# Kernel optimization log

Measured on AMD Instinct MI355X. Metric: run time of the kernel, lower is better.

Reference implementation:

```python
import jax, jax.numpy as jnp
import numpy as np

HIDDEN = 768
HEADS = 12
HEAD_DIM = HIDDEN // HEADS
BETA = 0.5
BANDWIDTH = 1.0
D_INTRINSIC = 3
LN_EPS = 1e-12


def setup_inputs() -> dict:
    key = jax.random.key(0)
    ks = jax.random.split(key, 10)
    B, S, E = 2, 2048, HIDDEN
    sc = 1.0 / np.sqrt(E)
    return {
        "hidden_states": jax.random.normal(ks[0], (B, S, E), jnp.float32),
        "attention_mask": jnp.zeros((B, S), jnp.float32),
        "Wq": jax.random.normal(ks[1], (E, E), jnp.float32) * sc,
        "bq": jax.random.normal(ks[2], (E,), jnp.float32) * 0.02,
        "Wv": jax.random.normal(ks[3], (E, E), jnp.float32) * sc,
        "bv": jax.random.normal(ks[4], (E,), jnp.float32) * 0.02,
        "Wo": jax.random.normal(ks[5], (E, E), jnp.float32) * sc,
        "bo": jax.random.normal(ks[6], (E,), jnp.float32) * 0.02,
        "ln_g": jnp.ones((E,), jnp.float32),
        "ln_b": jnp.zeros((E,), jnp.float32),
    }


def _layernorm(x, g, b, eps=LN_EPS):
    mu = jnp.mean(x, axis=-1, keepdims=True)
    var = jnp.mean((x - mu) ** 2, axis=-1, keepdims=True)
    return (x - mu) * jax.lax.rsqrt(var + eps) * g + b


def reference(hidden_states, attention_mask, Wq, bq, Wv, bv, Wo, bo, ln_g, ln_b):
    B, S, E = hidden_states.shape
    H, D = HEADS, HEAD_DIM
    # projections (torch Linear: x @ W.T + b)
    q = (hidden_states @ Wq.T + bq).reshape(B, S, H, D).transpose(0, 2, 1, 3)  # [B,H,S,D]
    v = (hidden_states @ Wv.T + bv).reshape(B, S, H, D).transpose(0, 2, 1, 3)  # [B,H,S,D]
    # pairwise Euclidean distance (cdist) via norm expansion, safe sqrt
    qn = jnp.sum(q * q, axis=-1)  # [B,H,S]
    d2 = qn[:, :, :, None] + qn[:, :, None, :] - 2.0 * jnp.einsum("bhid,bhjd->bhij", q, q)
    dist = jnp.sqrt(jnp.maximum(d2, 1e-12))  # [B,H,S,S]
    # mask: positions with attention_mask < 0 get distance 2
    keep = (attention_mask >= 0)  # [B,S]
    pair_keep = keep[:, None, :, None] & keep[:, None, None, :]  # [B,1,S,S]
    dist = jnp.where(pair_keep, dist, 2.0)
    # power-law score + softmax
    attn_score = (1.0 + dist / (BANDWIDTH ** 0.5)) ** (-D_INTRINSIC - BETA)
    attn = jax.nn.softmax(attn_score, axis=-1)
    out = jnp.einsum("bhij,bhjd->bhid", attn, v)  # [B,H,S,D]
    out = out.transpose(0, 2, 1, 3).reshape(B, S, E)
    # ModelSelfOutput: dense + residual + LayerNorm (dropout=0, eval)
    out = out @ Wo.T + bo
    return _layernorm(out + hidden_states, ln_g, ln_b)
```

## Files before the change

### kernel.cpp

```cpp
#include <hip/hip_runtime.h>
#include <hip/hip_bf16.h>
#include <cstdint>
#include <cstddef>

#define S_LEN 2048
#define NH 12
#define HD 64
#define EDIM 768

typedef short bf16x8 __attribute__((ext_vector_type(8)));
typedef float f32x4  __attribute__((ext_vector_type(4)));
typedef float f32x2  __attribute__((ext_vector_type(2)));

__device__ __forceinline__ unsigned short f2bf(float f) {
    return __bfloat16_as_ushort(__float2bfloat16(f));
}
__device__ __forceinline__ float bf2f(unsigned short u) {
    union { unsigned int i; float f; } x;
    x.i = ((unsigned int)u) << 16;
    return x.f;
}
__device__ __forceinline__ float rsq_f32(float x) {
#if __has_builtin(__builtin_amdgcn_rsqf)
    return __builtin_amdgcn_rsqf(x);
#else
    return __builtin_amdgcn_rcpf(__builtin_amdgcn_sqrtf(x));
#endif
}

__global__ __launch_bounds__(256) void precast_kernel(
    const float* __restrict__ hs, const float* __restrict__ Wq,
    const float* __restrict__ Wv, const float* __restrict__ Wo,
    unsigned short* __restrict__ hsb, unsigned short* __restrict__ Wqvb,
    unsigned short* __restrict__ Wob)
{
    const int i4 = blockIdx.x * 256 + threadIdx.x;
    const float* src;
    unsigned short* dst;
    int rel;
    if (i4 < 786432)        { src = hs; dst = hsb;            rel = i4; }
    else if (i4 < 933888)   { src = Wq; dst = Wqvb;           rel = i4 - 786432; }
    else if (i4 < 1081344)  { src = Wv; dst = Wqvb + 589824;  rel = i4 - 933888; }
    else                    { src = Wo; dst = Wob;            rel = i4 - 1081344; }
    float4 v = ((const float4*)src)[rel];
    ushort4 o;
    o.x = f2bf(v.x); o.y = f2bf(v.y); o.z = f2bf(v.z); o.w = f2bf(v.w);
    ((ushort4*)dst)[rel] = o;
}

__global__ __launch_bounds__(256) void qv_gemm(
    const unsigned short* __restrict__ hsb, const unsigned short* __restrict__ Wqvb,
    const float* __restrict__ bq, const float* __restrict__ bv,
    unsigned short* __restrict__ Qb, unsigned short* __restrict__ Vt,
    float* __restrict__ qn)
{
    __shared__ __align__(16) unsigned short As[64][40];
    __shared__ __align__(16) unsigned short Bs[128][40];

    const int t  = threadIdx.x;
    const int m0 = blockIdx.y << 6;
    const int c0 = blockIdx.x << 7;
    const bool isQ = (c0 < EDIM);
    const float* bias = isQ ? bq : bv;
    const int cb = isQ ? c0 : (c0 - EDIM);

    const int w  = t >> 6;
    const int l  = t & 63;
    const int ll = l & 15;
    const int lq = l >> 4;
    const int wx = w & 1;
    const int wy = w >> 1;

    const int srowA = t & 63;
    const int skA   = (t >> 6) << 3;
    const int srowB = t & 127;
    const int skB   = (t >> 7) << 4;

    f32x4 acc[2][4];
#pragma unroll
    for (int m = 0; m < 2; m++)
#pragma unroll
        for (int n = 0; n < 4; n++) acc[m][n] = (f32x4){0.f, 0.f, 0.f, 0.f};

    for (int k0 = 0; k0 < EDIM; k0 += 32) {
        bf16x8 va  = *(const bf16x8*)(hsb  + (size_t)(m0 + srowA) * EDIM + k0 + skA);
        bf16x8 vb0 = *(const bf16x8*)(Wqvb + (size_t)(c0 + srowB) * EDIM + k0 + skB);
        bf16x8 vb1 = *(const bf16x8*)(Wqvb + (size_t)(c0 + srowB) * EDIM + k0 + skB + 8);
        __syncthreads();
        *(bf16x8*)&As[srowA][skA]     = va;
        *(bf16x8*)&Bs[srowB][skB]     = vb0;
        *(bf16x8*)&Bs[srowB][skB + 8] = vb1;
        __syncthreads();
        bf16x8 aF[2], bF[4];
#pragma unroll
        for (int m = 0; m < 2; m++)
            aF[m] = *(const bf16x8*)&As[(wy << 5) + (m << 4) + ll][lq << 3];
#pragma unroll
        for (int n = 0; n < 4; n++)
            bF[n] = *(const bf16x8*)&Bs[(wx << 6) + (n << 4) + ll][lq << 3];
#pragma unroll
        for (int m = 0; m < 2; m++)
#pragma unroll
            for (int n = 0; n < 4; n++)
                acc[m][n] = __builtin_amdgcn_mfma_f32_16x16x32_bf16(aF[m], bF[n], acc[m][n], 0, 0, 0);
    }

    const int hcol0 = cb + (wx << 6);
    const int h = hcol0 >> 6;
    const int rowbase = m0 + (wy << 5);
    const int b = rowbase >> 11;
    const int sbase = rowbase & 2047;

    if (isQ) {
#pragma unroll
        for (int m = 0; m < 2; m++) {
#pragma unroll
            for (int r = 0; r < 4; r++) {
                const int si = sbase + (m << 4) + (lq << 2) + r;
                unsigned short* qrow = Qb + ((size_t)(b * NH + h) * S_LEN + si) * HD;
                float qsq = 0.f;
#pragma unroll
                for (int n = 0; n < 4; n++) {
                    unsigned short u = f2bf(acc[m][n][r] + bias[hcol0 + (n << 4) + ll]);
                    qrow[(n << 4) + ll] = u;
                    float f = bf2f(u);
                    qsq += f * f;
                }
                qsq += __shfl_xor(qsq, 1);
                qsq += __shfl_xor(qsq, 2);
                qsq += __shfl_xor(qsq, 4);
                qsq += __shfl_xor(qsq, 8);
                if (ll == 0) qn[(b * NH + h) * S_LEN + si] = qsq;
            }
        }
    } else {
#pragma unroll
        for (int m = 0; m < 2; m++) {
            const int si = sbase + (m << 4) + (lq << 2);
#pragma unroll
            for (int n = 0; n < 4; n++) {
                ushort4 o;
                o.x = f2bf(acc[m][n][0] + bias[hcol0 + (n << 4) + ll]);
                o.y = f2bf(acc[m][n][1] + bias[hcol0 + (n << 4) + ll]);
                o.z = f2bf(acc[m][n][2] + bias[hcol0 + (n << 4) + ll]);
                o.w = f2bf(acc[m][n][3] + bias[hcol0 + (n << 4) + ll]);
                *(ushort4*)&Vt[((size_t)(b * NH + h) * HD + (n << 4) + ll) * S_LEN + si] = o;
            }
        }
    }
}

template<int CUR>
__device__ __forceinline__ void attn_tile32(
    int j0, int jn,
    const unsigned short* __restrict__ Qbase,
    const unsigned short* __restrict__ Vbase,
    const float* __restrict__ qnb, const float* __restrict__ mb,
    int ll, int lq,
    const bf16x8 (&aQ)[2][2],
    const f32x2 (&qni2)[2][2], const f32x2 (&keepi2)[2][2],
    const bf16x8& ones,
    f32x4 (&oacc)[2][4], f32x4 (&wacc)[2],
    bf16x8 (&nb0)[2], bf16x8 (&nb1)[2],
    bf16x8 (&vbuf)[2][4],
    float (&qnjv)[2][2], float (&kjm)[2][2],
    unsigned short (&Wt)[2][2][16][40])
{
    constexpr int PRV = CUR ^ 1;
    __builtin_amdgcn_wave_barrier();
#pragma unroll
    for (int m = 0; m < 4; m++)
        vbuf[CUR][m] = *(const bf16x8*)(Vbase + (size_t)((m << 4) + ll) * S_LEN + j0 + (lq << 3));
    f32x4 s[2][2];
#pragma unroll
    for (int s2 = 0; s2 < 2; s2++)
#pragma unroll
        for (int n = 0; n < 2; n++) {
            f32x4 c = (f32x4){0.f, 0.f, 0.f, 0.f};
            c = __builtin_amdgcn_mfma_f32_16x16x32_bf16(aQ[s2][0], nb0[n], c, 0, 0, 0);
            c = __builtin_amdgcn_mfma_f32_16x16x32_bf16(aQ[s2][1], nb1[n], c, 0, 0, 0);
            s[s2][n] = c;
        }
#pragma unroll
    for (int n = 0; n < 2; n++) {
        const unsigned short* bp = Qbase + (size_t)(jn + (n << 4) + ll) * HD + (lq << 3);
        nb0[n] = *(const bf16x8*)bp;
        nb1[n] = *(const bf16x8*)(bp + 32);
        int jc = jn + (n << 4) + ll;
        qnjv[PRV][n] = qnb[jc];
        kjm[PRV][n]  = (mb[jc] >= 0.f) ? 1.f : 0.f;
    }
#pragma unroll
    for (int s2 = 0; s2 < 2; s2++) {
        bf16x8 aP = *(const bf16x8*)&Wt[PRV][s2][ll][lq << 3];
#pragma unroll
        for (int m = 0; m < 4; m++)
            oacc[s2][m] = __builtin_amdgcn_mfma_f32_16x16x32_bf16(aP, vbuf[PRV][m], oacc[s2][m], 0, 0, 0);
        wacc[s2] = __builtin_amdgcn_mfma_f32_16x16x32_bf16(aP, ones, wacc[s2], 0, 0, 0);
    }
#pragma unroll
    for (int s2 = 0; s2 < 2; s2++)
#pragma unroll
        for (int n = 0; n < 2; n++) {
            const f32x2 qv = (f32x2)(qnjv[CUR][n]);
            const f32x2 kj = (f32x2)(kjm[CUR][n]);
#pragma unroll
            for (int pr = 0; pr < 2; pr++) {
                f32x2 sp = { s[s2][n][2*pr], s[s2][n][2*pr + 1] };
                f32x2 d2 = __builtin_elementwise_fma(sp, (f32x2)(-2.f), qni2[s2][pr] + qv);
                d2 = __builtin_elementwise_max(d2, (f32x2)(1e-12f));
                f32x2 dist = { __builtin_amdgcn_sqrtf(d2.x), __builtin_amdgcn_sqrtf(d2.y) };
                f32x2 km = keepi2[s2][pr] * kj;
                f32x2 x  = __builtin_elementwise_fma(km, dist + (f32x2)(-2.f), (f32x2)(3.f));
                f32x2 x2 = x * x;
                f32x2 x4 = x2 * x2;
                f32x2 x6 = x4 * x2;
                f32x2 x7 = x6 * x;
                f32x2 p  = { rsq_f32(x7.x), rsq_f32(x7.y) };
                f32x2 wv = __builtin_elementwise_fma(
                    __builtin_elementwise_fma(
                        __builtin_elementwise_fma(
                            __builtin_elementwise_fma((f32x2)(0.041666668f), p, (f32x2)(0.16666667f)),
                            p, (f32x2)(0.5f)),
                        p, (f32x2)(1.0f)),
                    p, (f32x2)(1.0f));
                union { float f; unsigned int u; } c0, c1;
                c0.f = wv.x; c1.f = wv.y;
                Wt[CUR][s2][(lq << 2) + 2*pr    ][(n << 4) + ll] = (unsigned short)((c0.u + 0x8000u) >> 16);
                Wt[CUR][s2][(lq << 2) + 2*pr + 1][(n << 4) + ll] = (unsigned short)((c1.u + 0x8000u) >> 16);
            }
        }
}

__global__ __launch_bounds__(128) void attn_kernel(
    const unsigned short* __restrict__ Qb, const unsigned short* __restrict__ Vt,
    const float* __restrict__ qn, const float* __restrict__ mask,
    unsigned short* __restrict__ AObf)
{
    __shared__ __align__(16) unsigned short Wt[2][2][2][16][40];

    const int t  = threadIdx.x;
    const int w  = t >> 6;
    const int l  = t & 63;
    const int ll = l & 15;
    const int lq = l >> 4;
    const int id = blockIdx.x;
    const int ib = id / 24;
    const int bh = id - ib * 24;
    const int b  = bh / NH;
    const int h  = bh - b * NH;
    const int iw = ib << 5;

    const unsigned short* Qbase = Qb + ((size_t)bh << 17);
    const unsigned short* Vbase = Vt + ((size_t)bh << 17);
    const float* qnb = qn + (bh << 11);
    const float* mb  = mask + (b << 11);

    unsigned short (&Wtw)[2][2][16][40] = Wt[w];

    const int tbase = w << 5;
    const int jb    = tbase << 5;

    bf16x8 aQ[2][2];
#pragma unroll
    for (int s2 = 0; s2 < 2; s2++) {
        const unsigned short* qp = Qbase + (size_t)(iw + (s2 << 4) + ll) * HD + (lq << 3);
        aQ[s2][0] = *(const bf16x8*)qp;
        aQ[s2][1] = *(const bf16x8*)(qp + 32);
    }

    f32x2 qni2[2][2], keepi2[2][2];
#pragma unroll
    for (int s2 = 0; s2 < 2; s2++)
#pragma unroll
        for (int pr = 0; pr < 2; pr++) {
            int r0 = iw + (s2 << 4) + (lq << 2) + 2*pr;
            qni2[s2][pr]   = (f32x2){ qnb[r0], qnb[r0 + 1] };
            keepi2[s2][pr] = (f32x2){ (mb[r0] >= 0.f) ? 1.f : 0.f,
                                      (mb[r0 + 1] >= 0.f) ? 1.f : 0.f };
        }

    bf16x8 ones;
#pragma unroll
    for (int i = 0; i < 8; i++) ones[i] = (short)0x3F80;

    f32x4 oacc[2][4];
#pragma unroll
    for (int s2 = 0; s2 < 2; s2++)
#pragma unroll
        for (int m = 0; m < 4; m++) oacc[s2][m] = (f32x4){0.f, 0.f, 0.f, 0.f};
    f32x4 wacc[2];
    wacc[0] = (f32x4){0.f, 0.f, 0.f, 0.f};
    wacc[1] = (f32x4){0.f, 0.f, 0.f, 0.f};

    bf16x8 nb0[2], nb1[2];
    float qnjv[2][2], kjm[2][2];
#pragma unroll
    for (int n = 0; n < 2; n++) {
        const unsigned short* bp = Qbase + (size_t)(jb + (n << 4) + ll) * HD + (lq << 3);
        nb0[n] = *(const bf16x8*)bp;
        nb1[n] = *(const bf16x8*)(bp + 32);
        int jc = jb + (n << 4) + ll;
        qnjv[0][n] = qnb[jc];
        kjm[0][n]  = (mb[jc] >= 0.f) ? 1.f : 0.f;
    }
    bf16x8 vbuf[2][4];

    {
#pragma unroll
        for (int m = 0; m < 4; m++)
            vbuf[0][m] = *(const bf16x8*)(Vbase + (size_t)((m << 4) + ll) * S_LEN + jb + (lq << 3));
        f32x4 s[2][2];
#pragma unroll
        for (int s2 = 0; s2 < 2; s2++)
#pragma unroll
            for (int n = 0; n < 2; n++) {
                f32x4 c = (f32x4){0.f, 0.f, 0.f, 0.f};
                c = __builtin_amdgcn_mfma_f32_16x16x32_bf16(aQ[s2][0], nb0[n], c, 0, 0, 0);
                c = __builtin_amdgcn_mfma_f32_16x16x32_bf16(aQ[s2][1], nb1[n], c, 0, 0, 0);
                s[s2][n] = c;
            }
#pragma unroll
        for (int n = 0; n < 2; n++) {
            const unsigned short* bp = Qbase + (size_t)(jb + 32 + (n << 4) + ll) * HD + (lq << 3);
            nb0[n] = *(const bf16x8*)bp;
            nb1[n] = *(const bf16x8*)(bp + 32);
            int jc = jb + 32 + (n << 4) + ll;
            qnjv[1][n] = qnb[jc];
            kjm[1][n]  = (mb[jc] >= 0.f) ? 1.f : 0.f;
        }
#pragma unroll
        for (int s2 = 0; s2 < 2; s2++)
#pragma unroll
            for (int n = 0; n < 2; n++) {
                const f32x2 qv = (f32x2)(qnjv[0][n]);
                const f32x2 kj = (f32x2)(kjm[0][n]);
#pragma unroll
                for (int pr = 0; pr < 2; pr++) {
                    f32x2 sp = { s[s2][n][2*pr], s[s2][n][2*pr + 1] };
                    f32x2 d2 = __builtin_elementwise_fma(sp, (f32x2)(-2.f), qni2[s2][pr] + qv);
                    d2 = __builtin_elementwise_max(d2, (f32x2)(1e-12f));
                    f32x2 dist = { __builtin_amdgcn_sqrtf(d2.x), __builtin_amdgcn_sqrtf(d2.y) };
                    f32x2 km = keepi2[s2][pr] * kj;
                    f32x2 x  = __builtin_elementwise_fma(km, dist + (f32x2)(-2.f), (f32x2)(3.f));
                    f32x2 x2 = x * x;
                    f32x2 x4 = x2 * x2;
                    f32x2 x6 = x4 * x2;
                    f32x2 x7 = x6 * x;
                    f32x2 p  = { rsq_f32(x7.x), rsq_f32(x7.y) };
                    f32x2 wv = __builtin_elementwise_fma(
                        __builtin_elementwise_fma(
                            __builtin_elementwise_fma(
                                __builtin_elementwise_fma((f32x2)(0.041666668f), p, (f32x2)(0.16666667f)),
                                p, (f32x2)(0.5f)),
                            p, (f32x2)(1.0f)),
                        p, (f32x2)(1.0f));
                    union { float f; unsigned int u; } c0, c1;
                    c0.f = wv.x; c1.f = wv.y;
                    Wtw[0][s2][(lq << 2) + 2*pr    ][(n << 4) + ll] = (unsigned short)((c0.u + 0x8000u) >> 16);
                    Wtw[0][s2][(lq << 2) + 2*pr + 1][(n << 4) + ll] = (unsigned short)((c1.u + 0x8000u) >> 16);
                }
            }
    }

    for (int tt = tbase + 1; tt <= tbase + 29; tt += 2) {
        attn_tile32<1>(tt << 5, (tt + 1) << 5, Qbase, Vbase, qnb, mb, ll, lq,
                       aQ, qni2, keepi2, ones, oacc, wacc, nb0, nb1, vbuf, qnjv, kjm, Wtw);
        attn_tile32<0>((tt + 1) << 5, (tt + 2) << 5, Qbase, Vbase, qnb, mb, ll, lq,
                       aQ, qni2, keepi2, ones, oacc, wacc, nb0, nb1, vbuf, qnjv, kjm, Wtw);
    }
    attn_tile32<1>((tbase + 31) << 5, 0, Qbase, Vbase, qnb, mb, ll, lq,
                   aQ, qni2, keepi2, ones, oacc, wacc, nb0, nb1, vbuf, qnjv, kjm, Wtw);

    __builtin_amdgcn_wave_barrier();
#pragma unroll
    for (int s2 = 0; s2 < 2; s2++) {
        bf16x8 aP = *(const bf16x8*)&Wtw[1][s2][ll][lq << 3];
#pragma unroll
        for (int m = 0; m < 4; m++)
            oacc[s2][m] = __builtin_amdgcn_mfma_f32_16x16x32_bf16(aP, vbuf[1][m], oacc[s2][m], 0, 0, 0);
        wacc[s2] = __builtin_amdgcn_mfma_f32_16x16x32_bf16(aP, ones, wacc[s2], 0, 0, 0);
    }

    float* red = (float*)Wt;
    __syncthreads();
    if (w == 1) {
        float* p = red + l;
#pragma unroll
        for (int s2 = 0; s2 < 2; s2++)
#pragma unroll
            for (int m = 0; m < 4; m++)
#pragma unroll
                for (int r = 0; r < 4; r++)
                    p[((((s2 << 2) + m) << 2) + r) << 6] = oacc[s2][m][r];
#pragma unroll
        for (int s2 = 0; s2 < 2; s2++)
#pragma unroll
            for (int r = 0; r < 4; r++)
                p[(32 + (s2 << 2) + r) << 6] = wacc[s2][r];
    }
    __syncthreads();
    if (w == 0) {
        float* p = red + l;
#pragma unroll
        for (int s2 = 0; s2 < 2; s2++)
#pragma unroll
            for (int m = 0; m < 4; m++)
#pragma unroll
                for (int r = 0; r < 4; r++)
                    oacc[s2][m][r] += p[((((s2 << 2) + m) << 2) + r) << 6];
#pragma unroll
        for (int s2 = 0; s2 < 2; s2++)
#pragma unroll
            for (int r = 0; r < 4; r++)
                wacc[s2][r] += p[(32 + (s2 << 2) + r) << 6];

#pragma unroll
        for (int s2 = 0; s2 < 2; s2++)
#pragma unroll
            for (int r = 0; r < 4; r++) {
                float inv = 1.0f / wacc[s2][r];
                const int row = iw + (s2 << 4) + (lq << 2) + r;
                unsigned short* dst = AObf + (size_t)((b << 11) + row) * EDIM + (h << 6);
#pragma unroll
                for (int m = 0; m < 4; m++)
                    dst[(m << 4) + ll] = f2bf(oacc[s2][m][r] * inv);
            }
    }
}

__global__ __launch_bounds__(256) void oproj_gemm(
    const unsigned short* __restrict__ AObf, const unsigned short* __restrict__ Wob,
    const float* __restrict__ bo, const float* __restrict__ hs,
    float* __restrict__ TMP)
{
    __shared__ __align__(16) unsigned short As[64][40];
    __shared__ __align__(16) unsigned short Bs[64][40];

    const int t  = threadIdx.x;
    const int m0 = blockIdx.y << 6;
    const int c0 = blockIdx.x << 6;

    const int w  = t >> 6;
    const int l  = t & 63;
    const int ll = l & 15;
    const int lq = l >> 4;
    const int wx = w & 1;
    const int wy = w >> 1;

    const int srow = t & 63;
    const int sk   = (t >> 6) << 3;

    f32x4 acc[2][2];
#pragma unroll
    for (int m = 0; m < 2; m++)
#pragma unroll
        for (int n = 0; n < 2; n++) acc[m][n] = (f32x4){0.f, 0.f, 0.f, 0.f};

    for (int k0 = 0; k0 < EDIM; k0 += 32) {
        bf16x8 va = *(const bf16x8*)(AObf + (size_t)(m0 + srow) * EDIM + k0 + sk);
        bf16x8 vb = *(const bf16x8*)(Wob  + (size_t)(c0 + srow) * EDIM + k0 + sk);
        __syncthreads();
        *(bf16x8*)&As[srow][sk] = va;
        *(bf16x8*)&Bs[srow][sk] = vb;
        __syncthreads();
        bf16x8 aF[2], bF[2];
#pragma unroll
        for (int m = 0; m < 2; m++)
            aF[m] = *(const bf16x8*)&As[(wy << 5) + (m << 4) + ll][lq << 3];
#pragma unroll
        for (int n = 0; n < 2; n++)
            bF[n] = *(const bf16x8*)&Bs[(wx << 5) + (n << 4) + ll][lq << 3];
#pragma unroll
        for (int m = 0; m < 2; m++)
#pragma unroll
            for (int n = 0; n < 2; n++)
                acc[m][n] = __builtin_amdgcn_mfma_f32_16x16x32_bf16(aF[m], bF[n], acc[m][n], 0, 0, 0);
    }

#pragma unroll
    for (int m = 0; m < 2; m++) {
#pragma unroll
        for (int r = 0; r < 4; r++) {
            const int row = m0 + (wy << 5) + (m << 4) + (lq << 2) + r;
#pragma unroll
            for (int n = 0; n < 2; n++) {
                const int col = c0 + (wx << 5) + (n << 4) + ll;
                TMP[(size_t)row * EDIM + col] =
                    acc[m][n][r] + bo[col] + hs[(size_t)row * EDIM + col];
            }
        }
    }
}

__global__ __launch_bounds__(256) void ln_kernel(
    const float* __restrict__ X, const float* __restrict__ g,
    const float* __restrict__ be, float* __restrict__ out)
{
    const int row = blockIdx.x;
    const int t = threadIdx.x;
    const float* x = X + (size_t)row * EDIM;

    float s = 0.f, sq = 0.f;
#pragma unroll
    for (int c = t; c < EDIM; c += 256) {
        float v = x[c];
        s += v; sq += v * v;
    }
#pragma unroll
    for (int m = 1; m < 64; m <<= 1) {
        s  += __shfl_xor(s, m);
        sq += __shfl_xor(sq, m);
    }
    __shared__ float ss[4], ssq[4];
    const int w = t >> 6;
    if ((t & 63) == 0) { ss[w] = s; ssq[w] = sq; }
    __syncthreads();
    s  = ss[0] + ss[1] + ss[2] + ss[3];
    sq = ssq[0] + ssq[1] + ssq[2] + ssq[3];
    const float mu  = s * (1.f / EDIM);
    const float var = sq * (1.f / EDIM) - mu * mu;
    const float rstd = 1.0f / sqrtf(var + 1e-12f);

#pragma unroll
    for (int c = t; c < EDIM; c += 256) {
        out[(size_t)row * EDIM + c] = (x[c] - mu) * rstd * g[c] + be[c];
    }
}

extern "C" void kernel_launch(void* const* d_in, const int* in_sizes, int n_in,
                              void* d_out, int out_size, void* d_ws, size_t ws_size,
                              hipStream_t stream) {
    const float* hs   = (const float*)d_in[0];
    const float* mask = (const float*)d_in[1];
    const float* Wq   = (const float*)d_in[2];
    const float* bq   = (const float*)d_in[3];
    const float* Wv   = (const float*)d_in[4];
    const float* bv   = (const float*)d_in[5];
    const float* Wo   = (const float*)d_in[6];
    const float* bo   = (const float*)d_in[7];
    const float* g    = (const float*)d_in[8];
    const float* be   = (const float*)d_in[9];

    char* w8 = (char*)d_ws;
    unsigned short* Qb   = (unsigned short*)(w8);
    unsigned short* Vt   = (unsigned short*)(w8 +  6291456);
    float*          qn   = (float*)        (w8 + 12582912);
    unsigned short* AObf = (unsigned short*)(w8 + 12779520);
    unsigned short* hsb  = (unsigned short*)(w8 + 19070976);
    unsigned short* Wqvb = (unsigned short*)(w8 + 25362432);
    unsigned short* Wob  = (unsigned short*)(w8 + 27721728);
    float*          TMP  = (float*)(w8);

    precast_kernel<<<dim3(4800),    256, 0, stream>>>(hs, Wq, Wv, Wo, hsb, Wqvb, Wob);
    qv_gemm       <<<dim3(12, 64),  256, 0, stream>>>(hsb, Wqvb, bq, bv, Qb, Vt, qn);
    attn_kernel   <<<dim3(1536),    128, 0, stream>>>(Qb, Vt, qn, mask, AObf);
    oproj_gemm    <<<dim3(12, 64),  256, 0, stream>>>(AObf, Wob, bo, hs, TMP);
    ln_kernel     <<<dim3(4096),    256, 0, stream>>>(TMP, g, be, (float*)d_out);
}
```

Before: 264.1 us.

## Split attention key range across four waves per block with two-stage reduction

Each attention block now runs 256 threads instead of 128, so the key dimension is split four ways across waves rather than two, and each wave processes half as many key tiles. Partial outputs and normalizer sums are then merged in two stages through shared memory: waves 2–3 into waves 0–1, then wave 1 into wave 0. The goal is more waves in flight per CU and a shorter serial tile loop per wave, to hide latency better. The cost is an extra reduction round with more barriers, plus larger register and LDS pressure per block.

Measured after the change: 250.5 us. 1.05x faster.

```diff
diff --git a/kernel.cpp b/kernel.cpp
--- a/kernel.cpp
+++ b/kernel.cpp
@@ -232,12 +232,12 @@
         }
 }
 
-__global__ __launch_bounds__(128) void attn_kernel(
+__global__ __launch_bounds__(256) void attn_kernel(
     const unsigned short* __restrict__ Qb, const unsigned short* __restrict__ Vt,
     const float* __restrict__ qn, const float* __restrict__ mask,
     unsigned short* __restrict__ AObf)
 {
-    __shared__ __align__(16) unsigned short Wt[2][2][2][16][40];
+    __shared__ __align__(16) unsigned short Wt[4][2][2][16][40];
 
     const int t  = threadIdx.x;
     const int w  = t >> 6;
@@ -258,7 +258,7 @@
 
     unsigned short (&Wtw)[2][2][16][40] = Wt[w];
 
-    const int tbase = w << 5;
+    const int tbase = w << 4;
     const int jb    = tbase << 5;
 
     bf16x8 aQ[2][2];
@@ -363,13 +363,13 @@
             }
     }
 
-    for (int tt = tbase + 1; tt <= tbase + 29; tt += 2) {
+    for (int tt = tbase + 1; tt <= tbase + 13; tt += 2) {
         attn_tile32<1>(tt << 5, (tt + 1) << 5, Qbase, Vbase, qnb, mb, ll, lq,
                        aQ, qni2, keepi2, ones, oacc, wacc, nb0, nb1, vbuf, qnjv, kjm, Wtw);
         attn_tile32<0>((tt + 1) << 5, (tt + 2) << 5, Qbase, Vbase, qnb, mb, ll, lq,
                        aQ, qni2, keepi2, ones, oacc, wacc, nb0, nb1, vbuf, qnjv, kjm, Wtw);
     }
-    attn_tile32<1>((tbase + 31) << 5, 0, Qbase, Vbase, qnb, mb, ll, lq,
+    attn_tile32<1>((tbase + 15) << 5, 0, Qbase, Vbase, qnb, mb, ll, lq,
                    aQ, qni2, keepi2, ones, oacc, wacc, nb0, nb1, vbuf, qnjv, kjm, Wtw);
 
     __builtin_amdgcn_wave_barrier();
@@ -384,6 +384,38 @@
 
     float* red = (float*)Wt;
     __syncthreads();
+    if (w >= 2) {
+        float* p = red + (((w - 2) << 6) + l);
+#pragma unroll
+        for (int s2 = 0; s2 < 2; s2++)
+#pragma unroll
+            for (int m = 0; m < 4; m++)
+#pragma unroll
+                for (int r = 0; r < 4; r++)
+                    p[((((s2 << 2) + m) << 2) + r) * 128] = oacc[s2][m][r];
+#pragma unroll
+        for (int s2 = 0; s2 < 2; s2++)
+#pragma unroll
+            for (int r = 0; r < 4; r++)
+                p[(32 + (s2 << 2) + r) * 128] = wacc[s2][r];
+    }
+    __syncthreads();
+    if (w < 2) {
+        float* p = red + ((w << 6) + l);
+#pragma unroll
+        for (int s2 = 0; s2 < 2; s2++)
+#pragma unroll
+            for (int m = 0; m < 4; m++)
+#pragma unroll
+                for (int r = 0; r < 4; r++)
+                    oacc[s2][m][r] += p[((((s2 << 2) + m) << 2) + r) * 128];
+#pragma unroll
+        for (int s2 = 0; s2 < 2; s2++)
+#pragma unroll
+            for (int r = 0; r < 4; r++)
+                wacc[s2][r] += p[(32 + (s2 << 2) + r) * 128];
+    }
+    __syncthreads();
     if (w == 1) {
         float* p = red + l;
 #pragma unroll
@@ -392,12 +424,12 @@
             for (int m = 0; m < 4; m++)
 #pragma unroll
                 for (int r = 0; r < 4; r++)
-                    p[((((s2 << 2) + m) << 2) + r) << 6] = oacc[s2][m][r];
+                    p[((((s2 << 2) + m) << 2) + r) * 128] = oacc[s2][m][r];
 #pragma unroll
         for (int s2 = 0; s2 < 2; s2++)
 #pragma unroll
             for (int r = 0; r < 4; r++)
-                p[(32 + (s2 << 2) + r) << 6] = wacc[s2][r];
+                p[(32 + (s2 << 2) + r) * 128] = wacc[s2][r];
     }
     __syncthreads();
     if (w == 0) {
@@ -408,12 +440,12 @@
             for (int m = 0; m < 4; m++)
 #pragma unroll
                 for (int r = 0; r < 4; r++)
-                    oacc[s2][m][r] += p[((((s2 << 2) + m) << 2) + r) << 6];
+                    oacc[s2][m][r] += p[((((s2 << 2) + m) << 2) + r) * 128];
 #pragma unroll
         for (int s2 = 0; s2 < 2; s2++)
 #pragma unroll
             for (int r = 0; r < 4; r++)
-                wacc[s2][r] += p[(32 + (s2 << 2) + r) << 6];
+                wacc[s2][r] += p[(32 + (s2 << 2) + r) * 128];
 
 #pragma unroll
         for (int s2 = 0; s2 < 2; s2++)
@@ -554,7 +586,7 @@
 
     precast_kernel<<<dim3(4800),    256, 0, stream>>>(hs, Wq, Wv, Wo, hsb, Wqvb, Wob);
     qv_gemm       <<<dim3(12, 64),  256, 0, stream>>>(hsb, Wqvb, bq, bv, Qb, Vt, qn);
-    attn_kernel   <<<dim3(1536),    128, 0, stream>>>(Qb, Vt, qn, mask, AObf);
+    attn_kernel   <<<dim3(1536),    256, 0, stream>>>(Qb, Vt, qn, mask, AObf);
     oproj_gemm    <<<dim3(12, 64),  256, 0, stream>>>(AObf, Wob, bo, hs, TMP);
     ln_kernel     <<<dim3(4096),    256, 0, stream>>>(TMP, g, be, (float*)d_out);
 }
```
